# Optimization experiments

Measured on AMD Instinct MI355X. Metric: run time of the kernel, lower is better.

Reference implementation:

```python
import jax, jax.numpy as jnp
import numpy as np

B, L, N, C = 64, 12, 4096, 3
FD, HD, OUT = 32, 64, 12
TID, DIW, TD = 288, 7, 16
STEPS = 4
EMB = 10  # node embedding dim for learned adjacency


def setup_inputs() -> dict:
    key = jax.random.key(0)
    ks = jax.random.split(key, 16)
    g = lambda i, shape, s=0.05: jax.random.normal(ks[i], shape, dtype=jnp.float32) * s
    z = lambda n: jnp.zeros((n,), jnp.float32)
    return {
        "history_data": jax.random.uniform(ks[0], (B, L, N, C), dtype=jnp.float32),
        "future_data": jnp.zeros((B, L, N, 1), jnp.float32),
        "batch_seen": 0,
        "epoch": 0,
        "train": 1,
        "tid_emb": g(1, (TID, TD)),
        "diw_emb": g(2, (DIW, TD)),
        "t2f_w": g(3, (2 * TD, FD)), "t2f_b": z(FD),
        "enc_w1": g(4, (L * C, HD)), "enc_b1": z(HD),
        "enc_w2": g(5, (HD, FD)), "enc_b2": z(FD),
        "node_emb": g(6, (N, EMB), 1.0),
        "pde_w1": g(7, (FD, HD)), "pde_b1": z(HD),
        "pde_w2": g(8, (HD, FD)), "pde_b2": z(FD),
        "ss_win": g(9, (FD, FD)), "ss_wst": g(10, (FD, FD)), "ss_b": z(FD),
        "ss_wout": g(11, (FD, FD)), "ss_bout": z(FD),
        "dec_w1": g(12, (FD, HD)), "dec_b1": z(HD),
        "dec_w2": g(13, (HD, OUT)), "dec_b2": z(OUT),
        "pde_mix": jnp.array(0.5, jnp.float32),
    }


def reference(history_data, future_data, batch_seen, epoch, train,
              tid_emb, diw_emb, t2f_w, t2f_b,
              enc_w1, enc_b1, enc_w2, enc_b2,
              node_emb,
              pde_w1, pde_b1, pde_w2, pde_b2,
              ss_win, ss_wst, ss_b, ss_wout, ss_bout,
              dec_w1, dec_b1, dec_w2, dec_b2, pde_mix):
    # --- encoder: per-node MLP over flattened (L, C) history ---
    x = history_data[..., :C]                                    # [B,L,N,C]
    x = jnp.transpose(x, (0, 2, 1, 3)).reshape(B, N, L * C)      # [B,N,L*C]
    field = jnp.maximum(x @ enc_w1 + enc_b1, 0.0) @ enc_w2 + enc_b2  # [B,N,FD]

    # --- temporal field bias from last-step tid/diw ---
    tid_idx = jnp.clip((history_data[:, -1, :, 1] * TID).astype(jnp.int32), 0, TID - 1)
    diw_idx = jnp.clip((history_data[:, -1, :, 2] * DIW).astype(jnp.int32), 0, DIW - 1)
    temp = jnp.concatenate([tid_emb[tid_idx], diw_emb[diw_idx]], axis=-1)  # [B,N,2*TD]
    field = field + temp @ t2f_w + t2f_b

    # --- learned adjacency for graph Laplacian (L = I - A) ---
    A = jax.nn.softmax(jnp.maximum(node_emb @ node_emb.T, 0.0), axis=-1)  # [N,N]

    alpha = jax.nn.sigmoid(pde_mix)
    dt = 1.0 / STEPS
    state = jnp.zeros_like(field)
    for _ in range(STEPS):  # fixed small unroll over PDE steps
        L_F = jnp.einsum('nm,bmf->bnf', A, field) - field         # (A - I) F
        N_F = jnp.maximum(field @ pde_w1 + pde_b1, 0.0) @ pde_w2 + pde_b2
        fe = field + (alpha * L_F + (1.0 - alpha) * N_F) * dt
        state = jnp.tanh(fe @ ss_win + state @ ss_wst + ss_b)     # state-space update
        field = fe + state @ ss_wout + ss_bout

    # --- decoder: per-node MLP to output horizon ---
    pred = jnp.maximum(field @ dec_w1 + dec_b1, 0.0) @ dec_w2 + dec_b2  # [B,N,OUT]
    return jnp.transpose(pred, (0, 2, 1))[..., None]              # [B,OUT,N,1]
```

## Files before the change

kernel.cpp:

```cpp
#include <hip/hip_runtime.h>

#define BATCH 64
#define LHIST 12
#define NNODE 4096
#define CCH   3
#define FD    32
#define HD    64
#define OUTD  12
#define TIDN  288
#define DIWN  7
#define TDD   16
#define EMBD  10
#define MROWS 2048
#define KDIM  4096
#define MTOT  (BATCH * NNODE)

typedef __attribute__((ext_vector_type(8))) short bf16x8;
typedef __attribute__((ext_vector_type(4))) float f32x4;

union BF8U { bf16x8 v; unsigned short s[8]; };

__device__ __forceinline__ unsigned short f2b(float f) {
    union { float f; unsigned u; } v; v.f = f;
    unsigned r = v.u + 0x7fffu + ((v.u >> 16) & 1u);
    return (unsigned short)(r >> 16);
}

__device__ __forceinline__ float b2f(unsigned short u) {
    union { unsigned u; float f; } v; v.u = (unsigned)u << 16; return v.f;
}

__device__ __forceinline__ float fast_tanh(float x) {
    x = fminf(fmaxf(x, -15.f), 15.f);
    const float e = __expf(2.f * x);
    return (e - 1.f) / (e + 1.f);
}

__device__ __forceinline__ void gl2lds16(const void* g, void* l) {
    __builtin_amdgcn_global_load_lds((__attribute__((address_space(1))) void*)(void*)g,
                                     (__attribute__((address_space(3))) void*)l, 16, 0, 0);
}

__device__ __forceinline__ bf16x8 ldsfrag(const unsigned short* p) {
    return *(const bf16x8*)p;
}

__device__ __forceinline__ bf16x8 pack8(float4 a, float4 b) {
    BF8U u;
    u.s[0] = f2b(a.x); u.s[1] = f2b(a.y); u.s[2] = f2b(a.z); u.s[3] = f2b(a.w);
    u.s[4] = f2b(b.x); u.s[5] = f2b(b.y); u.s[6] = f2b(b.z); u.s[7] = f2b(b.w);
    return u.v;
}

__global__ __launch_bounds__(256) void build_A(const float* __restrict__ emb,
                                               unsigned short* __restrict__ A) {
    const int n = blockIdx.x;
    const int tid = threadIdx.x;
    __shared__ float sc[NNODE];
    __shared__ float red[256];
    float e[EMBD];
#pragma unroll
    for (int c = 0; c < EMBD; c++) e[c] = emb[(size_t)n * EMBD + c];
    float mx = 0.f;
    for (int m = tid; m < NNODE; m += 256) {
        float s = 0.f;
#pragma unroll
        for (int c = 0; c < EMBD; c++) s += e[c] * emb[(size_t)m * EMBD + c];
        s = fmaxf(s, 0.f);
        sc[m] = s;
        mx = fmaxf(mx, s);
    }
    red[tid] = mx;
    __syncthreads();
    for (int off = 128; off > 0; off >>= 1) {
        if (tid < off) red[tid] = fmaxf(red[tid], red[tid + off]);
        __syncthreads();
    }
    mx = red[0];
    __syncthreads();
    float sum = 0.f;
    for (int m = tid; m < NNODE; m += 256) {
        float v = expf(sc[m] - mx);
        sc[m] = v;
        sum += v;
    }
    red[tid] = sum;
    __syncthreads();
    for (int off = 128; off > 0; off >>= 1) {
        if (tid < off) red[tid] += red[tid + off];
        __syncthreads();
    }
    const float inv = 1.f / red[0];
    for (int m = tid; m < NNODE; m += 256)
        A[(size_t)n * NNODE + m] = f2b(sc[m] * inv);
}

__global__ __launch_bounds__(256, 2) void encoder(const float* __restrict__ hist,
                                                  const float* __restrict__ tid_emb,
                                                  const float* __restrict__ diw_emb,
                                                  const float* __restrict__ t2f_w,
                                                  const float* __restrict__ t2f_b,
                                                  const float* __restrict__ enc_w1,
                                                  const float* __restrict__ enc_b1,
                                                  const float* __restrict__ enc_w2,
                                                  const float* __restrict__ enc_b2,
                                                  float* __restrict__ field,
                                                  unsigned short* __restrict__ fT) {
    const int gid = blockIdx.x * 256 + threadIdx.x;
    const int b = gid >> 12;
    const int n = gid & (NNODE - 1);
    const float* hb = hist + ((size_t)b * LHIST * NNODE + n) * CCH;
    float x[LHIST * CCH];
#pragma unroll
    for (int l = 0; l < LHIST; l++) {
        x[l * 3 + 0] = hb[(size_t)l * NNODE * CCH + 0];
        x[l * 3 + 1] = hb[(size_t)l * NNODE * CCH + 1];
        x[l * 3 + 2] = hb[(size_t)l * NNODE * CCH + 2];
    }
    float f[FD];
#pragma unroll
    for (int o = 0; o < FD; o++) f[o] = enc_b2[o] + t2f_b[o];
    for (int j = 0; j < HD; j++) {
        float h = enc_b1[j];
#pragma unroll
        for (int k = 0; k < LHIST * CCH; k++) h += x[k] * enc_w1[k * HD + j];
        h = fmaxf(h, 0.f);
#pragma unroll
        for (int o = 0; o < FD; o++) f[o] += h * enc_w2[j * FD + o];
    }
    const int ti = min(max((int)(x[11 * 3 + 1] * 288.0f), 0), TIDN - 1);
    const int di = min(max((int)(x[11 * 3 + 2] * 7.0f), 0), DIWN - 1);
    for (int g = 0; g < TDD; g++) {
        const float tg = tid_emb[ti * TDD + g];
        const float dg = diw_emb[di * TDD + g];
#pragma unroll
        for (int o = 0; o < FD; o++)
            f[o] += tg * t2f_w[g * FD + o] + dg * t2f_w[(TDD + g) * FD + o];
    }
#pragma unroll
    for (int o4 = 0; o4 < FD / 4; o4++) {
        float4 v = {f[o4 * 4 + 0], f[o4 * 4 + 1], f[o4 * 4 + 2], f[o4 * 4 + 3]};
        *(float4*)&field[(size_t)gid * FD + o4 * 4] = v;
    }
#pragma unroll
    for (int o = 0; o < FD; o++)
        fT[(size_t)(b * FD + o) * NNODE + n] = f2b(f[o]);
}

__global__ __launch_bounds__(256) void gemm_bt(const unsigned short* __restrict__ X,
                                               const unsigned short* __restrict__ Y,
                                               unsigned short* __restrict__ Cp) {
    constexpr int K = KDIM;
    constexpr int KS = KDIM / 2;
    constexpr int BK = 32;
    __shared__ __align__(16) unsigned short Xs[128 * BK];
    __shared__ __align__(16) unsigned short Ys[128 * BK];
    const int tid = threadIdx.x;
    const int wave = tid >> 6;
    const int lane = tid & 63;

    const int l = blockIdx.x + 16 * blockIdx.y;
    const int xcd = l & 7;
    const int rem = l >> 3;
    const int by = xcd * 4 + (rem & 3);
    const int bx = rem >> 2;
    const int i0 = bx * 128;
    const int j0 = by * 128;
    const int k0 = blockIdx.z * KS;
    unsigned short* C = Cp + (size_t)blockIdx.z * MTOT * FD;

    const int wi = (wave >> 1) * 64;
    const int wj = (wave & 1) * 64;

    const int lrow = lane >> 2;
    const int lcol = ((lane & 3) ^ ((lane >> 3) & 3)) * 8;

    const unsigned short* Xg = X + (size_t)(i0 + wave * 32 + lrow) * K + k0 + lcol;
    const unsigned short* Yg = Y + (size_t)(j0 + wave * 32 + lrow) * K + k0 + lcol;
    unsigned short* Xl0 = &Xs[(wave * 32) * BK];
    unsigned short* Xl1 = &Xs[(wave * 32 + 16) * BK];
    unsigned short* Yl0 = &Ys[(wave * 32) * BK];
    unsigned short* Yl1 = &Ys[(wave * 32 + 16) * BK];

    const f32x4 zero = {0.f, 0.f, 0.f, 0.f};
    f32x4 acc[4][4];
#pragma unroll
    for (int a = 0; a < 4; a++)
#pragma unroll
        for (int b = 0; b < 4; b++) acc[a][b] = zero;

    const int fr = lane & 15;
    const int q = lane >> 4;
    const int kq = (q ^ ((fr >> 1) & 3)) * 8;

    for (int kt = 0; kt < KS; kt += BK) {
        __syncthreads();
        gl2lds16(Xg + kt, Xl0);
        gl2lds16(Xg + kt + 16 * K, Xl1);
        gl2lds16(Yg + kt, Yl0);
        gl2lds16(Yg + kt + 16 * K, Yl1);
        __syncthreads();
        bf16x8 fa[4], fb[4];
#pragma unroll
        for (int t = 0; t < 4; t++)
            fa[t] = *(const bf16x8*)&Xs[(wi + t * 16 + fr) * BK + kq];
#pragma unroll
        for (int t = 0; t < 4; t++)
            fb[t] = *(const bf16x8*)&Ys[(wj + t * 16 + fr) * BK + kq];
#pragma unroll
        for (int mi = 0; mi < 4; mi++)
#pragma unroll
            for (int ni = 0; ni < 4; ni++)
                acc[mi][ni] = __builtin_amdgcn_mfma_f32_16x16x32_bf16(
                    fa[mi], fb[ni], acc[mi][ni], 0, 0, 0);
    }

    const int r0 = q * 4;
#pragma unroll
    for (int mi = 0; mi < 4; mi++) {
#pragma unroll
        for (int ni = 0; ni < 4; ni++) {
            const int R0 = i0 + wi + mi * 16 + r0;
            const int col = j0 + wj + ni * 16 + fr;
            const size_t addr = ((size_t)(R0 >> 5) * NNODE + col) * FD + (R0 & 31);
            ushort4 pk = {f2b(acc[mi][ni][0]), f2b(acc[mi][ni][1]),
                          f2b(acc[mi][ni][2]), f2b(acc[mi][ni][3])};
            *(ushort4*)&C[addr] = pk;
        }
    }
}

#define HPAD 72
#define FPAD 40
__global__ __launch_bounds__(256, 2) void step_mfma(const unsigned short* __restrict__ Ct0,
                                                    const unsigned short* __restrict__ Ct1,
                                                    float* __restrict__ field,
                                                    unsigned short* __restrict__ state,
                                                    unsigned short* __restrict__ fT,
                                                    const float* __restrict__ pde_w1,
                                                    const float* __restrict__ pde_b1,
                                                    const float* __restrict__ pde_w2,
                                                    const float* __restrict__ pde_b2,
                                                    const float* __restrict__ ss_win,
                                                    const float* __restrict__ ss_wst,
                                                    const float* __restrict__ ss_b,
                                                    const float* __restrict__ ss_wout,
                                                    const float* __restrict__ ss_bout,
                                                    const float* __restrict__ pde_mix,
                                                    int first) {
    __shared__ __align__(16) unsigned short W1T[HD * FD];
    __shared__ __align__(16) unsigned short W2T[FD * HD];
    __shared__ __align__(16) unsigned short WinT[FD * FD];
    __shared__ __align__(16) unsigned short WstT[FD * FD];
    __shared__ __align__(16) unsigned short WoutT[FD * FD];
    __shared__ __align__(16) unsigned short Hs[4 * 64 * HPAD];
    __shared__ __align__(16) unsigned short Fs[4 * 64 * FPAD];

    const int tid = threadIdx.x;
    for (int i = tid; i < HD * FD; i += 256) W1T[(i & 63) * FD + (i >> 6)] = f2b(pde_w1[i]);
    for (int i = tid; i < HD * FD; i += 256) W2T[(i & 31) * HD + (i >> 5)] = f2b(pde_w2[i]);
    for (int i = tid; i < FD * FD; i += 256) {
        WinT [(i & 31) * FD + (i >> 5)] = f2b(ss_win[i]);
        WstT [(i & 31) * FD + (i >> 5)] = f2b(ss_wst[i]);
        WoutT[(i & 31) * FD + (i >> 5)] = f2b(ss_wout[i]);
    }
    __syncthreads();

    const int wv = tid >> 6;
    const int lane = tid & 63;
    const int ln = lane & 15;
    const int q = lane >> 4;
    const int kq = q * 8;
    const int r0 = q * 4;
    const int mw = blockIdx.x * 256 + wv * 64;
    const int b = mw >> 12;
    const int n0 = mw & (NNODE - 1);
    unsigned short* Hw = &Hs[wv * 64 * HPAD];
    unsigned short* Fw = &Fs[wv * 64 * FPAD];

    const float alpha = 1.f / (1.f + __expf(-pde_mix[0]));
    const float dt = 0.25f;

    bf16x8 w1f[4], w2f[2][2], winf[2], wstf[2], woutf[2];
#pragma unroll
    for (int nj = 0; nj < 4; nj++) w1f[nj] = ldsfrag(&W1T[(nj * 16 + ln) * FD + kq]);
#pragma unroll
    for (int nf = 0; nf < 2; nf++) {
#pragma unroll
        for (int kk = 0; kk < 2; kk++)
            w2f[nf][kk] = ldsfrag(&W2T[(nf * 16 + ln) * HD + kk * 32 + kq]);
        winf[nf]  = ldsfrag(&WinT [(nf * 16 + ln) * FD + kq]);
        wstf[nf]  = ldsfrag(&WstT [(nf * 16 + ln) * FD + kq]);
        woutf[nf] = ldsfrag(&WoutT[(nf * 16 + ln) * FD + kq]);
    }

    float b1v[4], b2v[2], bsv[2], bov[2];
#pragma unroll
    for (int nj = 0; nj < 4; nj++) b1v[nj] = pde_b1[nj * 16 + ln];
#pragma unroll
    for (int nf = 0; nf < 2; nf++) {
        b2v[nf] = pde_b2[nf * 16 + ln];
        bsv[nf] = ss_b[nf * 16 + ln];
        bov[nf] = ss_bout[nf * 16 + ln];
    }

    bf16x8 fA[4], stA[4];
#pragma unroll
    for (int mi = 0; mi < 4; mi++) {
        const float4* fp = (const float4*)&field[(size_t)(mw + mi * 16 + ln) * FD + kq];
        fA[mi] = pack8(fp[0], fp[1]);
    }
    if (!first) {
#pragma unroll
        for (int mi = 0; mi < 4; mi++)
            stA[mi] = *(const bf16x8*)&state[(size_t)(mw + mi * 16 + ln) * FD + kq];
    }

    const f32x4 zero = {0.f, 0.f, 0.f, 0.f};

    f32x4 hc[4][4];
#pragma unroll
    for (int mi = 0; mi < 4; mi++)
#pragma unroll
        for (int nj = 0; nj < 4; nj++)
            hc[mi][nj] = __builtin_amdgcn_mfma_f32_16x16x32_bf16(fA[mi], w1f[nj], zero, 0, 0, 0);
#pragma unroll
    for (int mi = 0; mi < 4; mi++)
#pragma unroll
        for (int nj = 0; nj < 4; nj++)
#pragma unroll
            for (int r = 0; r < 4; r++)
                Hw[(mi * 16 + r0 + r) * HPAD + nj * 16 + ln] =
                    f2b(fmaxf(hc[mi][nj][r] + b1v[nj], 0.f));
    __syncthreads();

    float fld[4][2][4], ctv[4][2][4];
#pragma unroll
    for (int mi = 0; mi < 4; mi++)
#pragma unroll
        for (int nf = 0; nf < 2; nf++)
#pragma unroll
            for (int r = 0; r < 4; r++) {
                const size_t idx = (size_t)(mw + mi * 16 + r0 + r) * FD + nf * 16 + ln;
                fld[mi][nf][r] = field[idx];
                ctv[mi][nf][r] = b2f(Ct0[idx]) + b2f(Ct1[idx]);
            }

    bf16x8 hA[4][2];
#pragma unroll
    for (int mi = 0; mi < 4; mi++)
#pragma unroll
        for (int kk = 0; kk < 2; kk++)
            hA[mi][kk] = ldsfrag(&Hw[(mi * 16 + ln) * HPAD + kk * 32 + kq]);
    f32x4 nc[4][2];
#pragma unroll
    for (int mi = 0; mi < 4; mi++)
#pragma unroll
        for (int nf = 0; nf < 2; nf++) {
            f32x4 a = __builtin_amdgcn_mfma_f32_16x16x32_bf16(hA[mi][0], w2f[nf][0], zero, 0, 0, 0);
            nc[mi][nf] = __builtin_amdgcn_mfma_f32_16x16x32_bf16(hA[mi][1], w2f[nf][1], a, 0, 0, 0);
        }

    float fe[4][2][4];
#pragma unroll
    for (int mi = 0; mi < 4; mi++)
#pragma unroll
        for (int nf = 0; nf < 2; nf++)
#pragma unroll
            for (int r = 0; r < 4; r++) {
                const float nfv = nc[mi][nf][r] + b2v[nf];
                const float fv = fld[mi][nf][r];
                fe[mi][nf][r] = fv + (alpha * (ctv[mi][nf][r] - fv) + (1.f - alpha) * nfv) * dt;
                Fw[(mi * 16 + r0 + r) * FPAD + nf * 16 + ln] = f2b(fe[mi][nf][r]);
            }
    __syncthreads();

    bf16x8 feA[4];
#pragma unroll
    for (int mi = 0; mi < 4; mi++) feA[mi] = ldsfrag(&Fw[(mi * 16 + ln) * FPAD + kq]);
    f32x4 sc_[4][2];
#pragma unroll
    for (int mi = 0; mi < 4; mi++)
#pragma unroll
        for (int nf = 0; nf < 2; nf++) {
            f32x4 a = __builtin_amdgcn_mfma_f32_16x16x32_bf16(feA[mi], winf[nf], zero, 0, 0, 0);
            if (!first)
                a = __builtin_amdgcn_mfma_f32_16x16x32_bf16(stA[mi], wstf[nf], a, 0, 0, 0);
            sc_[mi][nf] = a;
        }
    float sval[4][2][4];
#pragma unroll
    for (int mi = 0; mi < 4; mi++)
#pragma unroll
        for (int nf = 0; nf < 2; nf++)
#pragma unroll
            for (int r = 0; r < 4; r++)
                sval[mi][nf][r] = fast_tanh(sc_[mi][nf][r] + bsv[nf]);
    __syncthreads();
#pragma unroll
    for (int mi = 0; mi < 4; mi++)
#pragma unroll
        for (int nf = 0; nf < 2; nf++)
#pragma unroll
            for (int r = 0; r < 4; r++)
                Fw[(mi * 16 + r0 + r) * FPAD + nf * 16 + ln] = f2b(sval[mi][nf][r]);
    __syncthreads();

    bf16x8 SA[4];
#pragma unroll
    for (int mi = 0; mi < 4; mi++) SA[mi] = ldsfrag(&Fw[(mi * 16 + ln) * FPAD + kq]);
#pragma unroll
    for (int mi = 0; mi < 4; mi++) {
#pragma unroll
        for (int nf = 0; nf < 2; nf++) {
            f32x4 oc = __builtin_amdgcn_mfma_f32_16x16x32_bf16(SA[mi], woutf[nf], zero, 0, 0, 0);
            float fnew[4];
#pragma unroll
            for (int r = 0; r < 4; r++) {
                fnew[r] = fe[mi][nf][r] + oc[r] + bov[nf];
                const size_t idx = (size_t)(mw + mi * 16 + r0 + r) * FD + nf * 16 + ln;
                field[idx] = fnew[r];
                state[idx] = f2b(sval[mi][nf][r]);
            }
            ushort4 pk = {f2b(fnew[0]), f2b(fnew[1]), f2b(fnew[2]), f2b(fnew[3])};
            const size_t ft_addr = (size_t)(b * FD + nf * 16 + ln) * NNODE + n0 + mi * 16 + r0;
            *(ushort4*)&fT[ft_addr] = pk;
        }
    }
}

__global__ __launch_bounds__(256, 2) void decoder(const float* __restrict__ field,
                                                  const float* __restrict__ dw1,
                                                  const float* __restrict__ db1,
                                                  const float* __restrict__ dw2,
                                                  const float* __restrict__ db2,
                                                  float* __restrict__ out) {
    const int gid = blockIdx.x * 256 + threadIdx.x;
    const int b = gid >> 12;
    const int n = gid & (NNODE - 1);
    float ff[FD];
#pragma unroll
    for (int o4 = 0; o4 < FD / 4; o4++) {
        float4 v = *(const float4*)&field[(size_t)gid * FD + o4 * 4];
        ff[o4 * 4 + 0] = v.x; ff[o4 * 4 + 1] = v.y; ff[o4 * 4 + 2] = v.z; ff[o4 * 4 + 3] = v.w;
    }
    float o[OUTD];
#pragma unroll
    for (int t = 0; t < OUTD; t++) o[t] = db2[t];
    for (int j = 0; j < HD; j++) {
        float h = db1[j];
#pragma unroll
        for (int k = 0; k < FD; k++) h += ff[k] * dw1[k * HD + j];
        h = fmaxf(h, 0.f);
#pragma unroll
        for (int t = 0; t < OUTD; t++) o[t] += h * dw2[j * OUTD + t];
    }
#pragma unroll
    for (int t = 0; t < OUTD; t++)
        out[(size_t)(b * OUTD + t) * NNODE + n] = o[t];
}

extern "C" void kernel_launch(void* const* d_in, const int* in_sizes, int n_in,
                              void* d_out, int out_size, void* d_ws, size_t ws_size,
                              hipStream_t stream) {
    (void)in_sizes; (void)n_in; (void)out_size; (void)ws_size;
    const float* hist    = (const float*)d_in[0];
    const float* tid_emb = (const float*)d_in[5];
    const float* diw_emb = (const float*)d_in[6];
    const float* t2f_w   = (const float*)d_in[7];
    const float* t2f_b   = (const float*)d_in[8];
    const float* enc_w1  = (const float*)d_in[9];
    const float* enc_b1  = (const float*)d_in[10];
    const float* enc_w2  = (const float*)d_in[11];
    const float* enc_b2  = (const float*)d_in[12];
    const float* node_emb= (const float*)d_in[13];
    const float* pde_w1  = (const float*)d_in[14];
    const float* pde_b1  = (const float*)d_in[15];
    const float* pde_w2  = (const float*)d_in[16];
    const float* pde_b2  = (const float*)d_in[17];
    const float* ss_win  = (const float*)d_in[18];
    const float* ss_wst  = (const float*)d_in[19];
    const float* ss_b    = (const float*)d_in[20];
    const float* ss_wout = (const float*)d_in[21];
    const float* ss_bout = (const float*)d_in[22];
    const float* dec_w1  = (const float*)d_in[23];
    const float* dec_b1  = (const float*)d_in[24];
    const float* dec_w2  = (const float*)d_in[25];
    const float* dec_b2  = (const float*)d_in[26];
    const float* pde_mix = (const float*)d_in[27];

    char* w = (char*)d_ws;
    unsigned short* A_bf = (unsigned short*)w;  w += (size_t)KDIM * KDIM * 2;
    unsigned short* fT   = (unsigned short*)w;  w += (size_t)MROWS * KDIM * 2;
    float* field = (float*)w;                   w += (size_t)MTOT * FD * 4;
    unsigned short* state = (unsigned short*)w; w += (size_t)MTOT * FD * 2;
    unsigned short* Cp    = (unsigned short*)w; w += (size_t)2 * MTOT * FD * 2;

    build_A<<<NNODE, 256, 0, stream>>>(node_emb, A_bf);
    encoder<<<(BATCH * NNODE) / 256, 256, 0, stream>>>(hist, tid_emb, diw_emb, t2f_w,
                                                       t2f_b, enc_w1, enc_b1, enc_w2,
                                                       enc_b2, field, fT);
    for (int s = 0; s < 4; s++) {
        gemm_bt<<<dim3(16, 32, 2), 256, 0, stream>>>(fT, A_bf, Cp);
        step_mfma<<<MTOT / 256, 256, 0, stream>>>(
            Cp, Cp + (size_t)MTOT * FD, field, state, fT, pde_w1, pde_b1, pde_w2,
            pde_b2, ss_win, ss_wst, ss_b, ss_wout, ss_bout, pde_mix, s == 0 ? 1 : 0);
    }
    decoder<<<(BATCH * NNODE) / 256, 256, 0, stream>>>(field, dec_w1, dec_b1, dec_w2,
                                                       dec_b2, (float*)d_out);
}
```

Measured before the change: 769.9 us.

## Double-buffer GEMM LDS tiles, fuse decoder into last step, drop per-wave syncs

The A-times-field GEMM changes from direct global-to-LDS loads with two barriers per k-tile to register-staged loads into double-buffered LDS, with one barrier per tile, so the next tile's global loads overlap the current tile's MFMAs. The decoder MLP is folded into the final step kernel and runs on MFMA, which removes a separate launch and the last field write and read. Several __syncthreads in step_mfma are removed because each wave works on its own LDS region. This adds register pressure and LDS use, and it relies on the per-wave LDS regions truly being private.

```diff
diff --git a/kernel.cpp b/kernel.cpp
--- a/kernel.cpp
+++ b/kernel.cpp
@@ -34,11 +34,6 @@
     x = fminf(fmaxf(x, -15.f), 15.f);
     const float e = __expf(2.f * x);
     return (e - 1.f) / (e + 1.f);
-}
-
-__device__ __forceinline__ void gl2lds16(const void* g, void* l) {
-    __builtin_amdgcn_global_load_lds((__attribute__((address_space(1))) void*)(void*)g,
-                                     (__attribute__((address_space(3))) void*)l, 16, 0, 0);
 }
 
 __device__ __forceinline__ bf16x8 ldsfrag(const unsigned short* p) {
@@ -153,8 +148,8 @@
     constexpr int K = KDIM;
     constexpr int KS = KDIM / 2;
     constexpr int BK = 32;
-    __shared__ __align__(16) unsigned short Xs[128 * BK];
-    __shared__ __align__(16) unsigned short Ys[128 * BK];
+    __shared__ __align__(16) unsigned short Xs[2][128 * BK];
+    __shared__ __align__(16) unsigned short Ys[2][128 * BK];
     const int tid = threadIdx.x;
     const int wave = tid >> 6;
     const int lane = tid & 63;
@@ -173,14 +168,13 @@
     const int wj = (wave & 1) * 64;
 
     const int lrow = lane >> 2;
-    const int lcol = ((lane & 3) ^ ((lane >> 3) & 3)) * 8;
-
-    const unsigned short* Xg = X + (size_t)(i0 + wave * 32 + lrow) * K + k0 + lcol;
-    const unsigned short* Yg = Y + (size_t)(j0 + wave * 32 + lrow) * K + k0 + lcol;
-    unsigned short* Xl0 = &Xs[(wave * 32) * BK];
-    unsigned short* Xl1 = &Xs[(wave * 32 + 16) * BK];
-    unsigned short* Yl0 = &Ys[(wave * 32) * BK];
-    unsigned short* Yl1 = &Ys[(wave * 32 + 16) * BK];
+    const int gcol = (lane & 3) * 8;
+    const int scol = ((lane & 3) ^ ((lane >> 3) & 3)) * 8;
+
+    const unsigned short* Xg = X + (size_t)(i0 + wave * 32 + lrow) * K + k0 + gcol;
+    const unsigned short* Yg = Y + (size_t)(j0 + wave * 32 + lrow) * K + k0 + gcol;
+    const int ldoff0 = (wave * 32 + lrow) * BK + scol;
+    const int ldoff1 = (wave * 32 + 16 + lrow) * BK + scol;
 
     const f32x4 zero = {0.f, 0.f, 0.f, 0.f};
     f32x4 acc[4][4];
@@ -193,26 +187,47 @@
     const int q = lane >> 4;
     const int kq = (q ^ ((fr >> 1) & 3)) * 8;
 
+    uint4 rx0 = *(const uint4*)(Xg);
+    uint4 rx1 = *(const uint4*)(Xg + 16 * K);
+    uint4 ry0 = *(const uint4*)(Yg);
+    uint4 ry1 = *(const uint4*)(Yg + 16 * K);
+    *(uint4*)&Xs[0][ldoff0] = rx0;
+    *(uint4*)&Xs[0][ldoff1] = rx1;
+    *(uint4*)&Ys[0][ldoff0] = ry0;
+    *(uint4*)&Ys[0][ldoff1] = ry1;
+    __syncthreads();
+
+    int p = 0;
     for (int kt = 0; kt < KS; kt += BK) {
-        __syncthreads();
-        gl2lds16(Xg + kt, Xl0);
-        gl2lds16(Xg + kt + 16 * K, Xl1);
-        gl2lds16(Yg + kt, Yl0);
-        gl2lds16(Yg + kt + 16 * K, Yl1);
-        __syncthreads();
+        const bool more = (kt + BK < KS);
+        if (more) {
+            rx0 = *(const uint4*)(Xg + kt + BK);
+            rx1 = *(const uint4*)(Xg + kt + BK + 16 * K);
+            ry0 = *(const uint4*)(Yg + kt + BK);
+            ry1 = *(const uint4*)(Yg + kt + BK + 16 * K);
+        }
         bf16x8 fa[4], fb[4];
 #pragma unroll
         for (int t = 0; t < 4; t++)
-            fa[t] = *(const bf16x8*)&Xs[(wi + t * 16 + fr) * BK + kq];
+            fa[t] = *(const bf16x8*)&Xs[p][(wi + t * 16 + fr) * BK + kq];
 #pragma unroll
         for (int t = 0; t < 4; t++)
-            fb[t] = *(const bf16x8*)&Ys[(wj + t * 16 + fr) * BK + kq];
+            fb[t] = *(const bf16x8*)&Ys[p][(wj + t * 16 + fr) * BK + kq];
 #pragma unroll
         for (int mi = 0; mi < 4; mi++)
 #pragma unroll
             for (int ni = 0; ni < 4; ni++)
                 acc[mi][ni] = __builtin_amdgcn_mfma_f32_16x16x32_bf16(
                     fa[mi], fb[ni], acc[mi][ni], 0, 0, 0);
+        if (more) {
+            const int np = p ^ 1;
+            *(uint4*)&Xs[np][ldoff0] = rx0;
+            *(uint4*)&Xs[np][ldoff1] = rx1;
+            *(uint4*)&Ys[np][ldoff0] = ry0;
+            *(uint4*)&Ys[np][ldoff1] = ry1;
+            __syncthreads();
+            p = np;
+        }
     }
 
     const int r0 = q * 4;
@@ -247,12 +262,19 @@
                                                     const float* __restrict__ ss_wout,
                                                     const float* __restrict__ ss_bout,
                                                     const float* __restrict__ pde_mix,
-                                                    int first) {
+                                                    const float* __restrict__ dec_w1,
+                                                    const float* __restrict__ dec_b1,
+                                                    const float* __restrict__ dec_w2,
+                                                    const float* __restrict__ dec_b2,
+                                                    float* __restrict__ out,
+                                                    int first, int last) {
     __shared__ __align__(16) unsigned short W1T[HD * FD];
     __shared__ __align__(16) unsigned short W2T[FD * HD];
     __shared__ __align__(16) unsigned short WinT[FD * FD];
     __shared__ __align__(16) unsigned short WstT[FD * FD];
     __shared__ __align__(16) unsigned short WoutT[FD * FD];
+    __shared__ __align__(16) unsigned short Wd1T[HD * FD];
+    __shared__ __align__(16) unsigned short Wd2T[16 * HD];
     __shared__ __align__(16) unsigned short Hs[4 * 64 * HPAD];
     __shared__ __align__(16) unsigned short Fs[4 * 64 * FPAD];
 
@@ -263,6 +285,14 @@
         WinT [(i & 31) * FD + (i >> 5)] = f2b(ss_win[i]);
         WstT [(i & 31) * FD + (i >> 5)] = f2b(ss_wst[i]);
         WoutT[(i & 31) * FD + (i >> 5)] = f2b(ss_wout[i]);
+    }
+    if (last) {
+        for (int i = tid; i < HD * FD; i += 256)
+            Wd1T[(i & 63) * FD + (i >> 6)] = f2b(dec_w1[i]);
+        for (int i = tid; i < 16 * HD; i += 256) {
+            const int o = i >> 6, j = i & 63;
+            Wd2T[i] = (o < OUTD) ? f2b(dec_w2[j * OUTD + o]) : (unsigned short)0;
+        }
     }
     __syncthreads();
 
@@ -332,7 +362,6 @@
             for (int r = 0; r < 4; r++)
                 Hw[(mi * 16 + r0 + r) * HPAD + nj * 16 + ln] =
                     f2b(fmaxf(hc[mi][nj][r] + b1v[nj], 0.f));
-    __syncthreads();
 
     float fld[4][2][4], ctv[4][2][4];
 #pragma unroll
@@ -373,7 +402,6 @@
                 fe[mi][nf][r] = fv + (alpha * (ctv[mi][nf][r] - fv) + (1.f - alpha) * nfv) * dt;
                 Fw[(mi * 16 + r0 + r) * FPAD + nf * 16 + ln] = f2b(fe[mi][nf][r]);
             }
-    __syncthreads();
 
     bf16x8 feA[4];
 #pragma unroll
@@ -396,7 +424,6 @@
 #pragma unroll
             for (int r = 0; r < 4; r++)
                 sval[mi][nf][r] = fast_tanh(sc_[mi][nf][r] + bsv[nf]);
-    __syncthreads();
 #pragma unroll
     for (int mi = 0; mi < 4; mi++)
 #pragma unroll
@@ -404,60 +431,90 @@
 #pragma unroll
             for (int r = 0; r < 4; r++)
                 Fw[(mi * 16 + r0 + r) * FPAD + nf * 16 + ln] = f2b(sval[mi][nf][r]);
-    __syncthreads();
 
     bf16x8 SA[4];
 #pragma unroll
     for (int mi = 0; mi < 4; mi++) SA[mi] = ldsfrag(&Fw[(mi * 16 + ln) * FPAD + kq]);
-#pragma unroll
-    for (int mi = 0; mi < 4; mi++) {
+    float fnew[4][2][4];
+#pragma unroll
+    for (int mi = 0; mi < 4; mi++)
 #pragma unroll
         for (int nf = 0; nf < 2; nf++) {
             f32x4 oc = __builtin_amdgcn_mfma_f32_16x16x32_bf16(SA[mi], woutf[nf], zero, 0, 0, 0);
-            float fnew[4];
-#pragma unroll
-            for (int r = 0; r < 4; r++) {
-                fnew[r] = fe[mi][nf][r] + oc[r] + bov[nf];
-                const size_t idx = (size_t)(mw + mi * 16 + r0 + r) * FD + nf * 16 + ln;
-                field[idx] = fnew[r];
-                state[idx] = f2b(sval[mi][nf][r]);
+#pragma unroll
+            for (int r = 0; r < 4; r++)
+                fnew[mi][nf][r] = fe[mi][nf][r] + oc[r] + bov[nf];
+        }
+
+    if (!last) {
+#pragma unroll
+        for (int mi = 0; mi < 4; mi++) {
+#pragma unroll
+            for (int nf = 0; nf < 2; nf++) {
+#pragma unroll
+                for (int r = 0; r < 4; r++) {
+                    const size_t idx = (size_t)(mw + mi * 16 + r0 + r) * FD + nf * 16 + ln;
+                    field[idx] = fnew[mi][nf][r];
+                    state[idx] = f2b(sval[mi][nf][r]);
+                }
+                ushort4 pk = {f2b(fnew[mi][nf][0]), f2b(fnew[mi][nf][1]),
+                              f2b(fnew[mi][nf][2]), f2b(fnew[mi][nf][3])};
+                const size_t ft_addr = (size_t)(b * FD + nf * 16 + ln) * NNODE + n0 + mi * 16 + r0;
+                *(ushort4*)&fT[ft_addr] = pk;
             }
-            ushort4 pk = {f2b(fnew[0]), f2b(fnew[1]), f2b(fnew[2]), f2b(fnew[3])};
-            const size_t ft_addr = (size_t)(b * FD + nf * 16 + ln) * NNODE + n0 + mi * 16 + r0;
-            *(ushort4*)&fT[ft_addr] = pk;
-        }
-    }
-}
-
-__global__ __launch_bounds__(256, 2) void decoder(const float* __restrict__ field,
-                                                  const float* __restrict__ dw1,
-                                                  const float* __restrict__ db1,
-                                                  const float* __restrict__ dw2,
-                                                  const float* __restrict__ db2,
-                                                  float* __restrict__ out) {
-    const int gid = blockIdx.x * 256 + threadIdx.x;
-    const int b = gid >> 12;
-    const int n = gid & (NNODE - 1);
-    float ff[FD];
-#pragma unroll
-    for (int o4 = 0; o4 < FD / 4; o4++) {
-        float4 v = *(const float4*)&field[(size_t)gid * FD + o4 * 4];
-        ff[o4 * 4 + 0] = v.x; ff[o4 * 4 + 1] = v.y; ff[o4 * 4 + 2] = v.z; ff[o4 * 4 + 3] = v.w;
-    }
-    float o[OUTD];
-#pragma unroll
-    for (int t = 0; t < OUTD; t++) o[t] = db2[t];
-    for (int j = 0; j < HD; j++) {
-        float h = db1[j];
-#pragma unroll
-        for (int k = 0; k < FD; k++) h += ff[k] * dw1[k * HD + j];
-        h = fmaxf(h, 0.f);
-#pragma unroll
-        for (int t = 0; t < OUTD; t++) o[t] += h * dw2[j * OUTD + t];
-    }
-#pragma unroll
-    for (int t = 0; t < OUTD; t++)
-        out[(size_t)(b * OUTD + t) * NNODE + n] = o[t];
+        }
+    } else {
+        bf16x8 wd1f[4], wd2f[2];
+#pragma unroll
+        for (int nj = 0; nj < 4; nj++) wd1f[nj] = ldsfrag(&Wd1T[(nj * 16 + ln) * FD + kq]);
+#pragma unroll
+        for (int kk = 0; kk < 2; kk++) wd2f[kk] = ldsfrag(&Wd2T[ln * HD + kk * 32 + kq]);
+        float db1v[4];
+#pragma unroll
+        for (int nj = 0; nj < 4; nj++) db1v[nj] = dec_b1[nj * 16 + ln];
+        const float db2v = (ln < OUTD) ? dec_b2[ln] : 0.f;
+
+#pragma unroll
+        for (int mi = 0; mi < 4; mi++)
+#pragma unroll
+            for (int nf = 0; nf < 2; nf++)
+#pragma unroll
+                for (int r = 0; r < 4; r++)
+                    Fw[(mi * 16 + r0 + r) * FPAD + nf * 16 + ln] = f2b(fnew[mi][nf][r]);
+        bf16x8 fnA[4];
+#pragma unroll
+        for (int mi = 0; mi < 4; mi++) fnA[mi] = ldsfrag(&Fw[(mi * 16 + ln) * FPAD + kq]);
+
+        f32x4 h2[4][4];
+#pragma unroll
+        for (int mi = 0; mi < 4; mi++)
+#pragma unroll
+            for (int nj = 0; nj < 4; nj++)
+                h2[mi][nj] = __builtin_amdgcn_mfma_f32_16x16x32_bf16(fnA[mi], wd1f[nj], zero, 0, 0, 0);
+#pragma unroll
+        for (int mi = 0; mi < 4; mi++)
+#pragma unroll
+            for (int nj = 0; nj < 4; nj++)
+#pragma unroll
+                for (int r = 0; r < 4; r++)
+                    Hw[(mi * 16 + r0 + r) * HPAD + nj * 16 + ln] =
+                        f2b(fmaxf(h2[mi][nj][r] + db1v[nj], 0.f));
+        bf16x8 h2A[4][2];
+#pragma unroll
+        for (int mi = 0; mi < 4; mi++)
+#pragma unroll
+            for (int kk = 0; kk < 2; kk++)
+                h2A[mi][kk] = ldsfrag(&Hw[(mi * 16 + ln) * HPAD + kk * 32 + kq]);
+#pragma unroll
+        for (int mi = 0; mi < 4; mi++) {
+            f32x4 a = __builtin_amdgcn_mfma_f32_16x16x32_bf16(h2A[mi][0], wd2f[0], zero, 0, 0, 0);
+            a = __builtin_amdgcn_mfma_f32_16x16x32_bf16(h2A[mi][1], wd2f[1], a, 0, 0, 0);
+            if (ln < OUTD) {
+                float4 v = {a[0] + db2v, a[1] + db2v, a[2] + db2v, a[3] + db2v};
+                *(float4*)&out[(size_t)(b * OUTD + ln) * NNODE + n0 + mi * 16 + r0] = v;
+            }
+        }
+    }
 }
 
 extern "C" void kernel_launch(void* const* d_in, const int* in_sizes, int n_in,
@@ -504,8 +561,8 @@
         gemm_bt<<<dim3(16, 32, 2), 256, 0, stream>>>(fT, A_bf, Cp);
         step_mfma<<<MTOT / 256, 256, 0, stream>>>(
             Cp, Cp + (size_t)MTOT * FD, field, state, fT, pde_w1, pde_b1, pde_w2,
-            pde_b2, ss_win, ss_wst, ss_b, ss_wout, ss_bout, pde_mix, s == 0 ? 1 : 0);
-    }
-    decoder<<<(BATCH * NNODE) / 256, 256, 0, stream>>>(field, dec_w1, dec_b1, dec_w2,
-                                                       dec_b2, (float*)d_out);
-}
+            pde_b2, ss_win, ss_wst, ss_b, ss_wout, ss_bout, pde_mix,
+            dec_w1, dec_b1, dec_w2, dec_b2, (float*)d_out,
+            s == 0 ? 1 : 0, s == 3 ? 1 : 0);
+    }
+}
```

Result: faster. 732.0 us (-4.9%).
